# Optimization experiments

Measured on AMD Instinct MI355X. Metric: run time of the kernel, lower is better.

Reference implementation:

```python
import jax, jax.numpy as jnp
import numpy as np

N = 2_000_000
C = 64
B = 16
H = C // 2  # reduction_ratio = 2


def setup_inputs() -> dict:
    key = jax.random.key(0)
    k1, k2, k3, k4, k5, k6 = jax.random.split(key, 6)
    x = jax.random.normal(k1, (N, C), dtype=jnp.float32)
    batch_ids = jnp.sort(jax.random.randint(k2, (N,), 0, B, dtype=jnp.int32))
    # nn.Linear-style params: y = x @ W.T + b
    W1 = jax.random.normal(k3, (H, C), dtype=jnp.float32) * (1.0 / np.sqrt(C))
    b1 = jax.random.normal(k4, (H,), dtype=jnp.float32) * 0.01
    W2 = jax.random.normal(k5, (C, H), dtype=jnp.float32) * (1.0 / np.sqrt(H))
    b2 = jax.random.normal(k6, (C,), dtype=jnp.float32) * 0.01
    return {"x": x, "batch_ids": batch_ids, "W1": W1, "b1": b1, "W2": W2, "b2": b2}


def reference(x, batch_ids, W1, b1, W2, b2):
    # Global avg / max pooling per batch segment -> [B, C]
    sums = jax.ops.segment_sum(x, batch_ids, num_segments=B)
    counts = jax.ops.segment_sum(jnp.ones((x.shape[0],), x.dtype), batch_ids, num_segments=B)
    avg = sums / jnp.maximum(counts, 1.0)[:, None]
    mx = jax.ops.segment_max(x, batch_ids, num_segments=B)

    def mlp(h):  # shared tiny MLP: Linear -> ReLU -> Linear
        return jax.nn.relu(h @ W1.T + b1) @ W2.T + b2

    att = jax.nn.sigmoid(mlp(avg) + mlp(mx))  # [B, C]
    # per-point broadcast multiply-add: x * att[batch] + x
    return x * att[batch_ids] + x
```

## Files before the change

### kernel.cpp

```cpp
#include <hip/hip_runtime.h>
#include <math.h>

#define NCH   64
#define NBAT  16
#define NHID  32
#define NBLK  1024

typedef float f4 __attribute__((ext_vector_type(4)));


__device__ __forceinline__ void atomicMaxF(float* addr, float v) {
    if (v >= 0.0f) atomicMax((int*)addr, __float_as_int(v));
    else           atomicMin((unsigned int*)addr, __float_as_uint(v));
}

__device__ __forceinline__ f4 vmax4(f4 a, f4 b) {
    f4 r;
    r.x = fmaxf(a.x, b.x); r.y = fmaxf(a.y, b.y);
    r.z = fmaxf(a.z, b.z); r.w = fmaxf(a.w, b.w);
    return r;
}

__device__ __forceinline__ int lower_bound_i(const int* __restrict__ a, int n, int v) {
    int lo = 0, hi = n;
    while (lo < hi) {
        const int mid = (lo + hi) >> 1;
        if (a[mid] < v) lo = mid + 1; else hi = mid;
    }
    return lo;
}

__global__ __launch_bounds__(256) void init_kernel(float* ws) {
    const int i = blockIdx.x * blockDim.x + threadIdx.x;
    if (i < 1024) {
        ws[i] = 0.0f;
        ws[1024 + i] = -INFINITY;
    }
}

__global__ __launch_bounds__(256) void pool_kernel(const float* __restrict__ x,
                                                   const int* __restrict__ bid,
                                                   float* __restrict__ wsum,
                                                   float* __restrict__ wmax,
                                                   int n, int rpb) {
    __shared__ int sstart[NBAT + 1];
    __shared__ f4 ls[256];
    __shared__ f4 lm[256];
    const int t = threadIdx.x;
    if (t <= NBAT) sstart[t] = (t == NBAT) ? n : lower_bound_i(bid, n, t);
    __syncthreads();

    const int c4 = t & 15;
    const int rg = t >> 4;
    const int r0 = blockIdx.x * rpb;
    const int rend = min(r0 + rpb, n);
    const f4 fzero = {0.f, 0.f, 0.f, 0.f};
    const f4 fninf = {-INFINITY, -INFINITY, -INFINITY, -INFINITY};

    for (int b = 0; b < NBAT; ++b) {
        const int lo = max(sstart[b], r0);
        const int hi = min(sstart[b + 1], rend);
        if (lo >= hi) continue;

        f4 s = fzero, m = fninf;
        const int base = lo + rg;
        const int k = (hi > base) ? ((hi - base + 15) >> 4) : 0;
        const float* xp = x + (size_t)base * NCH + c4 * 4;
        int j = 0;
        for (; j + 4 <= k; j += 4) {
            const f4 v0 = *reinterpret_cast<const f4*>(xp + (size_t)(j + 0) * 16 * NCH);
            const f4 v1 = *reinterpret_cast<const f4*>(xp + (size_t)(j + 1) * 16 * NCH);
            const f4 v2 = *reinterpret_cast<const f4*>(xp + (size_t)(j + 2) * 16 * NCH);
            const f4 v3 = *reinterpret_cast<const f4*>(xp + (size_t)(j + 3) * 16 * NCH);
            s += v0; s += v1; s += v2; s += v3;
            m = vmax4(m, vmax4(vmax4(v0, v1), vmax4(v2, v3)));
        }
        for (; j < k; ++j) {
            const f4 v = *reinterpret_cast<const f4*>(xp + (size_t)j * 16 * NCH);
            s += v; m = vmax4(m, v);
        }

        ls[t] = s; lm[t] = m;
        __syncthreads();
        if (rg == 0) {
            for (int gg = 1; gg < 16; ++gg) {
                s += ls[gg * 16 + c4];
                m = vmax4(m, lm[gg * 16 + c4]);
            }
            float* ps = wsum + b * NCH + c4 * 4;
            atomicAdd(ps + 0, s.x);
            atomicAdd(ps + 1, s.y);
            atomicAdd(ps + 2, s.z);
            atomicAdd(ps + 3, s.w);
            float* pm = wmax + b * NCH + c4 * 4;
            atomicMaxF(pm + 0, m.x);
            atomicMaxF(pm + 1, m.y);
            atomicMaxF(pm + 2, m.z);
            atomicMaxF(pm + 3, m.w);
        }
        __syncthreads();
    }
}

__global__ __launch_bounds__(512) void mlp_kernel(const float* __restrict__ ws,
                                                  const int* __restrict__ bid,
                                                  const float* __restrict__ W1,
                                                  const float* __restrict__ b1,
                                                  const float* __restrict__ W2,
                                                  const float* __restrict__ b2,
                                                  float* __restrict__ scale_out,
                                                  int n) {
    __shared__ int   sstart[NBAT + 1];
    __shared__ float avg[NBAT * NCH];
    __shared__ float mxs[NBAT * NCH];
    __shared__ float h1a[NBAT * NHID];
    __shared__ float h1m[NBAT * NHID];
    const int t = threadIdx.x;
    if (t <= NBAT) sstart[t] = (t == NBAT) ? n : lower_bound_i(bid, n, t);
    __syncthreads();

    for (int i = t; i < NBAT * NCH; i += 512) {
        const int b = i >> 6;
        const float c = (float)(sstart[b + 1] - sstart[b]);
        avg[i] = ws[i] / fmaxf(c, 1.0f);
        mxs[i] = ws[1024 + i];
    }
    __syncthreads();

    {
        const int b = t >> 5, j = t & 31;
        float sa = b1[j], sm = b1[j];
        const float* w = W1 + j * NCH;
        for (int c = 0; c < NCH; ++c) {
            const float wv = w[c];
            sa += avg[b * NCH + c] * wv;
            sm += mxs[b * NCH + c] * wv;
        }
        h1a[b * NHID + j] = fmaxf(sa, 0.0f);
        h1m[b * NHID + j] = fmaxf(sm, 0.0f);
    }
    __syncthreads();

    for (int i = t; i < NBAT * NCH; i += 512) {
        const int b = i >> 6, c = i & 63;
        float ya = b2[c], ym = b2[c];
        const float* w = W2 + c * NHID;
        for (int j = 0; j < NHID; ++j) {
            const float wv = w[j];
            ya += h1a[b * NHID + j] * wv;
            ym += h1m[b * NHID + j] * wv;
        }
        const float z = ya + ym;
        const float sig = 1.0f / (1.0f + expf(-z));
        scale_out[i] = 1.0f + sig;
    }
}

__global__ __launch_bounds__(256) void apply_kernel(const float* __restrict__ x,
                                                    const int* __restrict__ bid,
                                                    const float* __restrict__ scale,
                                                    float* __restrict__ out,
                                                    int n, int rpb) {
    __shared__ int   sstart[NBAT + 1];
    __shared__ float s_scale[NBAT * NCH];
    const int t = threadIdx.x;
    if (t <= NBAT) sstart[t] = (t == NBAT) ? n : lower_bound_i(bid, n, t);
    for (int i = t; i < NBAT * NCH; i += 256) s_scale[i] = scale[i];
    __syncthreads();

    const int c4 = t & 15;
    const int rg = t >> 4;
    const int r0 = blockIdx.x * rpb;
    const int rend = min(r0 + rpb, n);

    for (int b = NBAT - 1; b >= 0; --b) {
        const int lo = max(sstart[b], r0);
        const int hi = min(sstart[b + 1], rend);
        if (lo >= hi) continue;

        const f4 sc = *reinterpret_cast<const f4*>(s_scale + b * NCH + c4 * 4);
        const int base = lo + rg;
        int k = (hi > base) ? ((hi - base + 15) >> 4) : 0;
        const float* xp = x + (size_t)base * NCH + c4 * 4;
        float* op = out + (size_t)base * NCH + c4 * 4;

        while (k >= 4) {
            k -= 4;
            const f4 v0 = *reinterpret_cast<const f4*>(xp + (size_t)(k + 0) * 16 * NCH);
            const f4 v1 = *reinterpret_cast<const f4*>(xp + (size_t)(k + 1) * 16 * NCH);
            const f4 v2 = *reinterpret_cast<const f4*>(xp + (size_t)(k + 2) * 16 * NCH);
            const f4 v3 = *reinterpret_cast<const f4*>(xp + (size_t)(k + 3) * 16 * NCH);
            __builtin_nontemporal_store(v0 * sc, reinterpret_cast<f4*>(op + (size_t)(k + 0) * 16 * NCH));
            __builtin_nontemporal_store(v1 * sc, reinterpret_cast<f4*>(op + (size_t)(k + 1) * 16 * NCH));
            __builtin_nontemporal_store(v2 * sc, reinterpret_cast<f4*>(op + (size_t)(k + 2) * 16 * NCH));
            __builtin_nontemporal_store(v3 * sc, reinterpret_cast<f4*>(op + (size_t)(k + 3) * 16 * NCH));
        }
        while (k > 0) {
            --k;
            const f4 v = *reinterpret_cast<const f4*>(xp + (size_t)k * 16 * NCH);
            __builtin_nontemporal_store(v * sc, reinterpret_cast<f4*>(op + (size_t)k * 16 * NCH));
        }
    }
}

extern "C" void kernel_launch(void* const* d_in, const int* in_sizes, int n_in,
                              void* d_out, int out_size, void* d_ws, size_t ws_size,
                              hipStream_t stream) {
    const float* x   = (const float*)d_in[0];
    const int*   bid = (const int*)d_in[1];
    const float* W1  = (const float*)d_in[2];
    const float* b1  = (const float*)d_in[3];
    const float* W2  = (const float*)d_in[4];
    const float* b2  = (const float*)d_in[5];
    float* out = (float*)d_out;
    const int n = in_sizes[1];

    float* ws     = (float*)d_ws;
    float* wsum   = ws;
    float* wmax   = ws + 1024;
    float* wscale = ws + 2064;

    hipLaunchKernelGGL(init_kernel, dim3(4), dim3(256), 0, stream, ws);

    const int rpb = (n + NBLK - 1) / NBLK;
    hipLaunchKernelGGL(pool_kernel, dim3(NBLK), dim3(256), 0, stream,
                       x, bid, wsum, wmax, n, rpb);

    hipLaunchKernelGGL(mlp_kernel, dim3(1), dim3(512), 0, stream,
                       ws, bid, W1, b1, W2, b2, wscale, n);

    hipLaunchKernelGGL(apply_kernel, dim3(NBLK), dim3(256), 0, stream,
                       x, bid, wscale, out, n, rpb);
}
```

Before: 302.3 us.

## Fuse MLP into pool kernel via last-block election and split apply blocks

The pool kernel now increments a global counter after its atomics, and the last block to finish computes the tiny MLP and writes the scale vector. This removes the separate single-block MLP launch and the gap that launch adds between pooling and apply. The apply kernel launches twice as many blocks, each covering half of a pool block's row range, with the second half mapped to the lower block indices, apparently so recently pooled rows are read while still in cache. The cost is a serialized MLP tail on one block and a counter reset added to init.

```diff
diff --git a/kernel.cpp b/kernel.cpp
--- a/kernel.cpp
+++ b/kernel.cpp
@@ -36,16 +36,29 @@
         ws[i] = 0.0f;
         ws[1024 + i] = -INFINITY;
     }
+    if (i == 1100) *(int*)(ws + 2048) = 0;
 }
 
 __global__ __launch_bounds__(256) void pool_kernel(const float* __restrict__ x,
                                                    const int* __restrict__ bid,
-                                                   float* __restrict__ wsum,
-                                                   float* __restrict__ wmax,
+                                                   const float* __restrict__ W1,
+                                                   const float* __restrict__ b1,
+                                                   const float* __restrict__ W2,
+                                                   const float* __restrict__ b2,
+                                                   float* __restrict__ ws,
                                                    int n, int rpb) {
     __shared__ int sstart[NBAT + 1];
     __shared__ f4 ls[256];
     __shared__ f4 lm[256];
+    __shared__ float h1a[NBAT * NHID];
+    __shared__ float h1m[NBAT * NHID];
+    __shared__ int elected;
+
+    float* wsum = ws;
+    float* wmax = ws + 1024;
+    int*   done = (int*)(ws + 2048);
+    float* wscale = ws + 2064;
+
     const int t = threadIdx.x;
     if (t <= NBAT) sstart[t] = (t == NBAT) ? n : lower_bound_i(bid, n, t);
     __syncthreads();
@@ -100,35 +113,26 @@
         }
         __syncthreads();
     }
-}
-
-__global__ __launch_bounds__(512) void mlp_kernel(const float* __restrict__ ws,
-                                                  const int* __restrict__ bid,
-                                                  const float* __restrict__ W1,
-                                                  const float* __restrict__ b1,
-                                                  const float* __restrict__ W2,
-                                                  const float* __restrict__ b2,
-                                                  float* __restrict__ scale_out,
-                                                  int n) {
-    __shared__ int   sstart[NBAT + 1];
-    __shared__ float avg[NBAT * NCH];
-    __shared__ float mxs[NBAT * NCH];
-    __shared__ float h1a[NBAT * NHID];
-    __shared__ float h1m[NBAT * NHID];
-    const int t = threadIdx.x;
-    if (t <= NBAT) sstart[t] = (t == NBAT) ? n : lower_bound_i(bid, n, t);
-    __syncthreads();
-
-    for (int i = t; i < NBAT * NCH; i += 512) {
+
+    __threadfence();
+    if (t == 0) elected = (atomicAdd(done, 1) == (int)gridDim.x - 1);
+    __syncthreads();
+    if (!elected) return;
+
+    float* avg = (float*)ls;
+    float* mxs = (float*)lm;
+    for (int i = t; i < NBAT * NCH; i += 256) {
         const int b = i >> 6;
         const float c = (float)(sstart[b + 1] - sstart[b]);
-        avg[i] = ws[i] / fmaxf(c, 1.0f);
-        mxs[i] = ws[1024 + i];
-    }
-    __syncthreads();
-
-    {
-        const int b = t >> 5, j = t & 31;
+        const float sv = __hip_atomic_load(&wsum[i], __ATOMIC_RELAXED, __HIP_MEMORY_SCOPE_AGENT);
+        const float mv = __hip_atomic_load(&wmax[i], __ATOMIC_RELAXED, __HIP_MEMORY_SCOPE_AGENT);
+        avg[i] = sv / fmaxf(c, 1.0f);
+        mxs[i] = mv;
+    }
+    __syncthreads();
+
+    for (int j2 = t; j2 < NBAT * NHID; j2 += 256) {
+        const int b = j2 >> 5, j = j2 & 31;
         float sa = b1[j], sm = b1[j];
         const float* w = W1 + j * NCH;
         for (int c = 0; c < NCH; ++c) {
@@ -136,12 +140,12 @@
             sa += avg[b * NCH + c] * wv;
             sm += mxs[b * NCH + c] * wv;
         }
-        h1a[b * NHID + j] = fmaxf(sa, 0.0f);
-        h1m[b * NHID + j] = fmaxf(sm, 0.0f);
-    }
-    __syncthreads();
-
-    for (int i = t; i < NBAT * NCH; i += 512) {
+        h1a[j2] = fmaxf(sa, 0.0f);
+        h1m[j2] = fmaxf(sm, 0.0f);
+    }
+    __syncthreads();
+
+    for (int i = t; i < NBAT * NCH; i += 256) {
         const int b = i >> 6, c = i & 63;
         float ya = b2[c], ym = b2[c];
         const float* w = W2 + c * NHID;
@@ -152,7 +156,7 @@
         }
         const float z = ya + ym;
         const float sig = 1.0f / (1.0f + expf(-z));
-        scale_out[i] = 1.0f + sig;
+        wscale[i] = 1.0f + sig;
     }
 }
 
@@ -160,7 +164,7 @@
                                                     const int* __restrict__ bid,
                                                     const float* __restrict__ scale,
                                                     float* __restrict__ out,
-                                                    int n, int rpb) {
+                                                    int n, int rpb, int hrs) {
     __shared__ int   sstart[NBAT + 1];
     __shared__ float s_scale[NBAT * NCH];
     const int t = threadIdx.x;
@@ -168,10 +172,12 @@
     for (int i = t; i < NBAT * NCH; i += 256) s_scale[i] = scale[i];
     __syncthreads();
 
+    const int pc   = blockIdx.x & (NBLK - 1);
+    const int half = 1 - (int)(blockIdx.x >> 10);
+    const int r0   = pc * rpb + half * hrs;
+    const int rend = min(min(pc * rpb + (half + 1) * hrs, pc * rpb + rpb), n);
     const int c4 = t & 15;
     const int rg = t >> 4;
-    const int r0 = blockIdx.x * rpb;
-    const int rend = min(r0 + rpb, n);
 
     for (int b = NBAT - 1; b >= 0; --b) {
         const int lo = max(sstart[b], r0);
@@ -216,19 +222,15 @@
     const int n = in_sizes[1];
 
     float* ws     = (float*)d_ws;
-    float* wsum   = ws;
-    float* wmax   = ws + 1024;
     float* wscale = ws + 2064;
 
-    hipLaunchKernelGGL(init_kernel, dim3(4), dim3(256), 0, stream, ws);
+    hipLaunchKernelGGL(init_kernel, dim3(8), dim3(256), 0, stream, ws);
 
     const int rpb = (n + NBLK - 1) / NBLK;
     hipLaunchKernelGGL(pool_kernel, dim3(NBLK), dim3(256), 0, stream,
-                       x, bid, wsum, wmax, n, rpb);
-
-    hipLaunchKernelGGL(mlp_kernel, dim3(1), dim3(512), 0, stream,
-                       ws, bid, W1, b1, W2, b2, wscale, n);
-
-    hipLaunchKernelGGL(apply_kernel, dim3(NBLK), dim3(256), 0, stream,
-                       x, bid, wscale, out, n, rpb);
-}
+                       x, bid, W1, b1, W2, b2, ws, n, rpb);
+
+    const int hrs = (rpb + 1) >> 1;
+    hipLaunchKernelGGL(apply_kernel, dim3(2 * NBLK), dim3(256), 0, stream,
+                       x, bid, wscale, out, n, rpb, hrs);
+}
```

Result: slower. 393.6 us (+30.2%).
